# Performance work log

Measured on AMD Instinct MI355X. Metric: run time of the kernel, lower is better.

## Reference

```python
import jax, jax.numpy as jnp
import numpy as np

B, N_NODES, D, H, L, DFF, K = 16, 512, 256, 8, 4, 1024, 128
DH = D // H


def setup_inputs() -> dict:
    key = jax.random.key(0)
    ks = jax.random.split(key, 16)
    x = jax.random.normal(ks[0], (B, N_NODES, D), jnp.float32)
    d = jax.random.uniform(ks[1], (B, N_NODES, N_NODES), jnp.float32)
    dist = 0.5 * (d + jnp.swapaxes(d, -1, -2))
    dist = dist * (1.0 - jnp.eye(N_NODES, dtype=jnp.float32))  # zero diagonal
    mask = jnp.ones((B, 1, N_NODES), dtype=bool)
    s = 0.02
    Wq = jax.random.normal(ks[2], (L, D, D), jnp.float32) * s
    Wk = jax.random.normal(ks[3], (L, D, D), jnp.float32) * s
    Wv = jax.random.normal(ks[4], (L, D, D), jnp.float32) * s
    Wo = jax.random.normal(ks[5], (L, D, D), jnp.float32) * s
    W1 = jax.random.normal(ks[6], (L, D, DFF), jnp.float32) * s
    W2 = jax.random.normal(ks[7], (L, DFF, D), jnp.float32) * s
    ln1_g = jnp.ones((L, D), jnp.float32)
    ln1_b = jnp.zeros((L, D), jnp.float32)
    ln2_g = jnp.ones((L, D), jnp.float32)
    ln2_b = jnp.zeros((L, D), jnp.float32)
    gamma = jnp.ones((D,), jnp.float32)
    beta = jnp.zeros((D,), jnp.float32)
    return dict(x=x, dist=dist, mask=mask, Wq=Wq, Wk=Wk, Wv=Wv, Wo=Wo, W1=W1, W2=W2,
                ln1_g=ln1_g, ln1_b=ln1_b, ln2_g=ln2_g, ln2_b=ln2_b, gamma=gamma, beta=beta)


def _ln(x, g, b, eps=1e-6):
    mu = jnp.mean(x, axis=-1, keepdims=True)
    var = jnp.mean((x - mu) ** 2, axis=-1, keepdims=True)
    return (x - mu) * jax.lax.rsqrt(var + eps) * g + b


def _afps(scores, dist, k):
    # scores: [H, n, n] attention probs; dist: [n, n]; mask assumed all-True.
    s = jnp.sum(jnp.mean(scores, axis=0), axis=-2)            # [n] column sums
    d = dist / jnp.max(dist) + (s / jnp.max(s))[:, None] * 0.1  # [n, n]
    n = d.shape[0]
    mind0 = d[:, 0]                                            # min dist to {0}
    sel0 = jnp.zeros((n,), bool).at[0].set(True)

    def body(carry, _):
        mind, sel = carry
        cand = jnp.where(sel, -jnp.inf, mind)  # exclude already-selected
        new = jnp.argmax(cand)
        return (jnp.minimum(mind, d[:, new]), sel.at[new].set(True)), new

    _, picks = jax.lax.scan(body, (mind0, sel0), None, length=k - 1)
    return jnp.concatenate([jnp.zeros((1,), picks.dtype), picks])  # [k]


def reference(x, dist, mask, Wq, Wk, Wv, Wo, W1, W2, ln1_g, ln1_b, ln2_g, ln2_b, gamma, beta):
    key_mask = mask[:, :, None, :]  # [B,1,1,n] broadcast over heads/queries
    inv_sqrt = np.float32(1.0 / np.sqrt(DH))
    scores = None
    for i in range(L):
        h = _ln(x, ln1_g[i], ln1_b[i])
        q = (h @ Wq[i]).reshape(B, N_NODES, H, DH).transpose(0, 2, 1, 3)
        kk = (h @ Wk[i]).reshape(B, N_NODES, H, DH).transpose(0, 2, 1, 3)
        v = (h @ Wv[i]).reshape(B, N_NODES, H, DH).transpose(0, 2, 1, 3)
        logits = jnp.einsum('bhqd,bhkd->bhqk', q, kk) * inv_sqrt - dist[:, None]
        logits = jnp.where(key_mask, logits, jnp.float32(-1e9))
        scores = jax.nn.softmax(logits, axis=-1)               # [B,H,n,n]
        attn = jnp.einsum('bhqk,bhkd->bhqd', scores, v)
        x = x + attn.transpose(0, 2, 1, 3).reshape(B, N_NODES, D) @ Wo[i]
        h2 = _ln(x, ln2_g[i], ln2_b[i])
        x = x + jax.nn.gelu(h2 @ W1[i]) @ W2[i]
    # AFPS index selection runs under no_grad in the original
    idx = jax.vmap(lambda sc, dd: _afps(sc, dd, K))(
        jax.lax.stop_gradient(scores), jax.lax.stop_gradient(dist))  # [B,K]
    pooled = jnp.mean(jnp.take_along_axis(x, idx[:, :, None], axis=1), axis=1)  # [B,D]
    return _ln(pooled, gamma, beta)
```

## Files before the change

### kernel.cpp

```cpp
#include <hip/hip_runtime.h>
#include <hip/hip_bf16.h>
#include <math.h>

#define BB 16
#define NN 512
#define DD 256
#define HH 8
#define LL 4
#define DFF 1024
#define KSEL 128
#define DH 32

typedef __attribute__((ext_vector_type(8))) short bf16x8v;
typedef __attribute__((ext_vector_type(4))) float f32x4v;

static const size_t X_B    = 0;
static const size_t QKVB_B = 8388608;
static const size_t VT_B   = 20971520;
static const size_t FFN_B  = 8388608;
static const size_t H_B    = 25165824;
static const size_t ATT_B  = 29360128;
static const size_t WQKV_B = 33554432;
static const size_t WO_B   = 35127296;
static const size_t W1T_B  = 35651584;
static const size_t W2T_B  = 37748736;
static const size_t S_B    = 39845888;
static const size_t MAXD_B = 39878656;
static const size_t IDX_B  = 39878720;

__device__ __forceinline__ float gelu_f(float x) {
  float x3 = x * x * x;
  return 0.5f * x * (1.f + tanhf(0.7978845608028654f * (x + 0.044715f * x3)));
}

__device__ __forceinline__ short bf16raw(float v) {
  __hip_bfloat16 h = __float2bfloat16(v);
  return *reinterpret_cast<short*>(&h);
}

__device__ __forceinline__ float blk_sum_256(float v, float* stmp) {
  #pragma unroll
  for (int o = 32; o > 0; o >>= 1) v += __shfl_down(v, o, 64);
  if ((threadIdx.x & 63) == 0) stmp[threadIdx.x >> 6] = v;
  __syncthreads();
  if (threadIdx.x == 0) stmp[0] = stmp[0] + stmp[1] + stmp[2] + stmp[3];
  __syncthreads();
  float r = stmp[0];
  __syncthreads();
  return r;
}

template <int CTRL>
__device__ __forceinline__ unsigned long long dpp_mov_u64(unsigned long long x) {
  int lo = __builtin_amdgcn_update_dpp(0, (int)(unsigned)x, CTRL, 0xf, 0xf, true);
  int hi = __builtin_amdgcn_update_dpp(0, (int)(unsigned)(x >> 32), CTRL, 0xf, 0xf, true);
  return ((unsigned long long)(unsigned)hi << 32) | (unsigned)lo;
}

__device__ __forceinline__ void merge_top2(unsigned long long& b1, unsigned long long& b2,
                                           unsigned long long n1, unsigned long long n2) {
  if (n1 > b1) {
    b2 = (b1 > n2) ? b1 : n2;
    b1 = n1;
  } else {
    b2 = (b2 > n1) ? b2 : n1;
  }
}


__global__ __launch_bounds__(256) void cast_weights_kernel(
    const float* __restrict__ Wq, const float* __restrict__ Wk,
    const float* __restrict__ Wv, const float* __restrict__ Wo,
    const float* __restrict__ W1, const float* __restrict__ W2,
    __hip_bfloat16* __restrict__ qkvT, __hip_bfloat16* __restrict__ WoT,
    __hip_bfloat16* __restrict__ W1T, __hip_bfloat16* __restrict__ W2T) {
  int i = blockIdx.x * 256 + threadIdx.x;
  if (i < 786432) {
    int l = i / 196608, r = i % 196608;
    int n = r >> 8, k = r & 255;
    const float* src = (n < 256) ? Wq : (n < 512 ? Wk : Wv);
    qkvT[i] = __float2bfloat16(src[l * 65536 + k * 256 + (n & 255)]);
  } else if (i < 1048576) {
    int j = i - 786432;
    int l = j >> 16, r = j & 65535;
    int n = r >> 8, k = r & 255;
    WoT[j] = __float2bfloat16(Wo[l * 65536 + k * 256 + n]);
  } else if (i < 2097152) {
    int j = i - 1048576;
    int l = j >> 18, r = j & 262143;
    int n = r >> 8, k = r & 255;
    W1T[j] = __float2bfloat16(W1[l * 262144 + k * 1024 + n]);
  } else {
    int j = i - 2097152;
    int l = j >> 18, r = j & 262143;
    int n = r >> 10, k = r & 1023;
    W2T[j] = __float2bfloat16(W2[l * 262144 + k * 256 + n]);
  }
}

__global__ __launch_bounds__(256) void ln_cast_kernel(const float* __restrict__ in,
                                                      const float* __restrict__ g,
                                                      const float* __restrict__ bb,
                                                      __hip_bfloat16* __restrict__ out) {
  const int tid = threadIdx.x;
  const int lane = tid & 63;
  const size_t row = (size_t)blockIdx.x * 4 + (tid >> 6);
  const float4 v = *(const float4*)(in + row * DD + lane * 4);
  float s1 = v.x + v.y + v.z + v.w;
  #pragma unroll
  for (int o = 32; o > 0; o >>= 1) s1 += __shfl_xor(s1, o, 64);
  const float mu = s1 * (1.f / DD);
  const float d0 = v.x - mu, d1 = v.y - mu, d2 = v.z - mu, d3 = v.w - mu;
  float s2 = d0 * d0 + d1 * d1 + d2 * d2 + d3 * d3;
  #pragma unroll
  for (int o = 32; o > 0; o >>= 1) s2 += __shfl_xor(s2, o, 64);
  const float rsig = rsqrtf(s2 * (1.f / DD) + 1e-6f);
  const float4 gg = *(const float4*)(g + lane * 4);
  const float4 bv = *(const float4*)(bb + lane * 4);
  short4 o;
  o.x = bf16raw(d0 * rsig * gg.x + bv.x);
  o.y = bf16raw(d1 * rsig * gg.y + bv.y);
  o.z = bf16raw(d2 * rsig * gg.z + bv.z);
  o.w = bf16raw(d3 * rsig * gg.w + bv.w);
  *(short4*)((short*)out + row * DD + lane * 4) = o;
}

template <int MODE>
__global__ __launch_bounds__(256) void mfma_gemm(const __hip_bfloat16* __restrict__ A,
                                                 const __hip_bfloat16* __restrict__ Bt,
                                                 void* __restrict__ Cv,
                                                 __hip_bfloat16* __restrict__ Vto,
                                                 int M, int N, int Kd) {
  __shared__ short As[64 * 40];
  __shared__ short Bs[64 * 40];
  const int tid = threadIdx.x;
  const int w = tid >> 6, lane = tid & 63;
  const int m16 = lane & 15, quad = lane >> 4;
  const int bm = blockIdx.y << 6, bn = blockIdx.x << 6;
  const int srow = tid >> 2, scol = (tid & 3) << 3;

  f32x4v acc[4];
  #pragma unroll
  for (int nt = 0; nt < 4; ++nt) acc[nt] = (f32x4v){0.f, 0.f, 0.f, 0.f};

  const short* Ag = (const short*)A;
  const short* Bg = (const short*)Bt;

  for (int k0 = 0; k0 < Kd; k0 += 32) {
    *(bf16x8v*)&As[srow * 40 + scol] =
        *(const bf16x8v*)(Ag + (size_t)(bm + srow) * Kd + k0 + scol);
    *(bf16x8v*)&Bs[srow * 40 + scol] =
        *(const bf16x8v*)(Bg + (size_t)(bn + srow) * Kd + k0 + scol);
    __syncthreads();
    bf16x8v af = *(bf16x8v*)&As[(w * 16 + m16) * 40 + (quad << 3)];
    #pragma unroll
    for (int nt = 0; nt < 4; ++nt) {
      bf16x8v bf = *(bf16x8v*)&Bs[(nt * 16 + m16) * 40 + (quad << 3)];
      acc[nt] = __builtin_amdgcn_mfma_f32_16x16x32_bf16(af, bf, acc[nt], 0, 0, 0);
    }
    __syncthreads();
  }

  const int erow = bm + w * 16 + quad * 4;
  #pragma unroll
  for (int nt = 0; nt < 4; ++nt) {
    int col = bn + nt * 16 + m16;
    if (MODE == 3) {
      if (col < 512) {
        #pragma unroll
        for (int r = 0; r < 4; ++r)
          ((__hip_bfloat16*)Cv)[(size_t)(erow + r) * 768 + col] =
              __float2bfloat16(acc[nt][r]);
      } else {
        short4 pk;
        pk.x = bf16raw(acc[nt][0]); pk.y = bf16raw(acc[nt][1]);
        pk.z = bf16raw(acc[nt][2]); pk.w = bf16raw(acc[nt][3]);
        int bb2 = erow >> 9, key = erow & 511, dim = col - 512;
        *(short4*)((short*)Vto + (size_t)bb2 * 131072 + (size_t)dim * 512 + key) = pk;
      }
    } else {
      #pragma unroll
      for (int r = 0; r < 4; ++r)
        ((__hip_bfloat16*)Cv)[(size_t)(erow + r) * N + col] =
            __float2bfloat16(gelu_f(acc[nt][r]));
    }
  }
}

__device__ __forceinline__ void gemm_res_body(const __hip_bfloat16* __restrict__ A,
                                              const __hip_bfloat16* __restrict__ Bt,
                                              const float* __restrict__ Res,
                                              float* __restrict__ C,
                                              int N, int Kd, int bm,
                                              short* As, short* Bs) {
  const int tid = threadIdx.x;
  const int w = tid >> 6, lane = tid & 63;
  const int m16 = lane & 15, quad = lane >> 4;
  const int bn = blockIdx.x << 6;
  const int srow = tid >> 2, scol = (tid & 3) << 3;

  f32x4v acc[4];
  #pragma unroll
  for (int nt = 0; nt < 4; ++nt) acc[nt] = (f32x4v){0.f, 0.f, 0.f, 0.f};

  const short* Ag = (const short*)A;
  const short* Bg = (const short*)Bt;

  for (int k0 = 0; k0 < Kd; k0 += 32) {
    *(bf16x8v*)&As[srow * 40 + scol] =
        *(const bf16x8v*)(Ag + (size_t)(bm + srow) * Kd + k0 + scol);
    *(bf16x8v*)&Bs[srow * 40 + scol] =
        *(const bf16x8v*)(Bg + (size_t)(bn + srow) * Kd + k0 + scol);
    __syncthreads();
    bf16x8v af = *(bf16x8v*)&As[(w * 16 + m16) * 40 + (quad << 3)];
    #pragma unroll
    for (int nt = 0; nt < 4; ++nt) {
      bf16x8v bf = *(bf16x8v*)&Bs[(nt * 16 + m16) * 40 + (quad << 3)];
      acc[nt] = __builtin_amdgcn_mfma_f32_16x16x32_bf16(af, bf, acc[nt], 0, 0, 0);
    }
    __syncthreads();
  }

  const int erow = bm + w * 16 + quad * 4;
  #pragma unroll
  for (int nt = 0; nt < 4; ++nt) {
    int col = bn + nt * 16 + m16;
    #pragma unroll
    for (int r = 0; r < 4; ++r) {
      size_t off = (size_t)(erow + r) * N + col;
      C[off] = acc[nt][r] + Res[off];
    }
  }
}

__global__ __launch_bounds__(256) void mfma_gemm_res(const __hip_bfloat16* __restrict__ A,
                                                     const __hip_bfloat16* __restrict__ Bt,
                                                     const float* __restrict__ Res,
                                                     float* __restrict__ C,
                                                     int N, int Kd) {
  __shared__ short As[64 * 40];
  __shared__ short Bs[64 * 40];
  gemm_res_body(A, Bt, Res, C, N, Kd, blockIdx.y << 6, As, Bs);
}

__device__ void afps_wave(int b, int lane,
                          const float* __restrict__ dist,
                          const float* __restrict__ s,
                          const unsigned int* __restrict__ maxd,
                          int* __restrict__ idx_out) {
  const float* db = dist + (size_t)b * NN * NN;

  float sv[8];
  float ms = 0.f;
  #pragma unroll
  for (int r = 0; r < 8; ++r) {
    sv[r] = s[b * NN + r * 64 + lane];
    ms = fmaxf(ms, sv[r]);
  }
  #pragma unroll
  for (int o = 32; o > 0; o >>= 1) ms = fmaxf(ms, __shfl_xor(ms, o, 64));

  const float invmaxd = 1.0f / __uint_as_float(maxd[b]);
  float sn[8], mind[8];
  #pragma unroll
  for (int r = 0; r < 8; ++r) {
    sn[r] = (sv[r] / ms) * 0.1f;
    mind[r] = db[r * 64 + lane] * invmaxd + sn[r];
  }
  unsigned selm = (lane == 0) ? 1u : 0u;
  if (lane == 0) idx_out[b * KSEL + 0] = 0;

  int specIdx = -1;
  float sreg[8];

  for (int it = 1; it < KSEL; ++it) {
    unsigned long long b1 = 0ull, b2 = 0ull;
    #pragma unroll
    for (int r = 0; r < 8; ++r) {
      unsigned long long pk =
          ((selm >> r) & 1u) ? 0ull
            : (((unsigned long long)__float_as_uint(mind[r])) << 32) |
              (unsigned)(511 - (r * 64 + lane));
      if (pk > b1) { b2 = b1; b1 = pk; }
      else if (pk > b2) b2 = pk;
    }
    { unsigned long long n1 = dpp_mov_u64<0x111>(b1), n2 = dpp_mov_u64<0x111>(b2); merge_top2(b1, b2, n1, n2); }
    { unsigned long long n1 = dpp_mov_u64<0x112>(b1), n2 = dpp_mov_u64<0x112>(b2); merge_top2(b1, b2, n1, n2); }
    { unsigned long long n1 = dpp_mov_u64<0x114>(b1), n2 = dpp_mov_u64<0x114>(b2); merge_top2(b1, b2, n1, n2); }
    { unsigned long long n1 = dpp_mov_u64<0x118>(b1), n2 = dpp_mov_u64<0x118>(b2); merge_top2(b1, b2, n1, n2); }
    { unsigned long long n1 = dpp_mov_u64<0x142>(b1), n2 = dpp_mov_u64<0x142>(b2); merge_top2(b1, b2, n1, n2); }
    { unsigned long long n1 = dpp_mov_u64<0x143>(b1), n2 = dpp_mov_u64<0x143>(b2); merge_top2(b1, b2, n1, n2); }
    const unsigned w1 = (unsigned)__builtin_amdgcn_readlane((int)(unsigned)b1, 63);
    const unsigned w2 = (unsigned)__builtin_amdgcn_readlane((int)(unsigned)b2, 63);
    const int nw = 511 - (int)(w1 & 0x1ffu);
    const int sec = 511 - (int)(w2 & 0x1ffu);

    float rowv[8];
    if (nw == specIdx) {
      #pragma unroll
      for (int r = 0; r < 8; ++r) rowv[r] = sreg[r];
    } else {
      const float* row = db + (size_t)nw * NN;
      #pragma unroll
      for (int r = 0; r < 8; ++r) rowv[r] = row[r * 64 + lane];
    }
    {
      const float* srow = db + (size_t)sec * NN;
      #pragma unroll
      for (int r = 0; r < 8; ++r) sreg[r] = srow[r * 64 + lane];
      specIdx = sec;
    }
    if (lane == (nw & 63)) selm |= 1u << (nw >> 6);
    if (lane == 0) idx_out[b * KSEL + it] = nw;
    #pragma unroll
    for (int r = 0; r < 8; ++r)
      mind[r] = fminf(mind[r], fmaf(rowv[r], invmaxd, sn[r]));
  }
}

__global__ __launch_bounds__(256) void wo_gemm_afps(const __hip_bfloat16* __restrict__ A,
                                                    const __hip_bfloat16* __restrict__ Bt,
                                                    const float* __restrict__ Res,
                                                    float* __restrict__ C,
                                                    const float* __restrict__ dist,
                                                    const float* __restrict__ s,
                                                    const unsigned int* __restrict__ maxd,
                                                    int* __restrict__ idx_out) {
  __shared__ short As[64 * 40];
  __shared__ short Bs[64 * 40];
  if (blockIdx.y == 0) {
    const int b = blockIdx.x * 4 + (threadIdx.x >> 6);
    afps_wave(b, threadIdx.x & 63, dist, s, maxd, idx_out);
    return;
  }
  gemm_res_body(A, Bt, Res, C, DD, 256, (blockIdx.y - 1) << 6, As, Bs);
}

__global__ __launch_bounds__(512) void attn_kernel(const __hip_bfloat16* __restrict__ qkvb,
                                                   const __hip_bfloat16* __restrict__ vt,
                                                   const float* __restrict__ dist,
                                                   __hip_bfloat16* __restrict__ outg,
                                                   float* __restrict__ s_acc,
                                                   int accum) {
  __shared__ float Pf[8][16 * 36];
  const int tid = threadIdx.x;
  const int h = tid >> 6, lane = tid & 63;
  const int m16 = lane & 15, quad = lane >> 4;
  const int b = blockIdx.y;
  const int qbase = blockIdx.x * 16;
  const float scale = 0.17677669529663687f;
  const f32x4v zero = {0.f, 0.f, 0.f, 0.f};

  const short* qkvs = (const short*)qkvb;
  const short* vts = (const short*)vt + (size_t)b * 131072;
  float* Pw = Pf[h];

  bf16x8v qf = *(const bf16x8v*)(qkvs + ((size_t)(b * NN + qbase + m16)) * 768 + h * 32 + (quad << 3));

  int drow[4];
  #pragma unroll
  for (int r = 0; r < 4; ++r) drow[r] = (b * NN + qbase + quad * 4 + r) * NN;

  f32x4v accO0 = zero, accO1 = zero;
  float laccL[4] = {0.f, 0.f, 0.f, 0.f};

  for (int t0 = 0; t0 < NN; t0 += 32) {
    bf16x8v kf0 = *(const bf16x8v*)(qkvs + ((size_t)(b * NN + t0 + m16)) * 768 + 256 + h * 32 + (quad << 3));
    bf16x8v kf1 = *(const bf16x8v*)(qkvs + ((size_t)(b * NN + t0 + 16 + m16)) * 768 + 256 + h * 32 + (quad << 3));
    f32x4v s0 = __builtin_amdgcn_mfma_f32_16x16x32_bf16(qf, kf0, zero, 0, 0, 0);
    f32x4v s1 = __builtin_amdgcn_mfma_f32_16x16x32_bf16(qf, kf1, zero, 0, 0, 0);
    #pragma unroll
    for (int r = 0; r < 4; ++r) {
      float e0 = __expf(fmaf(s0[r], scale, -dist[drow[r] + t0 + m16]));
      float e1 = __expf(fmaf(s1[r], scale, -dist[drow[r] + t0 + 16 + m16]));
      laccL[r] += e0 + e1;
      Pw[(quad * 4 + r) * 36 + m16] = e0;
      Pw[(quad * 4 + r) * 36 + 16 + m16] = e1;
    }
    bf16x8v pfr;
    {
      const float* pr = &Pw[m16 * 36 + (quad << 3)];
      float4 pa = *(const float4*)pr;
      float4 pb = *(const float4*)(pr + 4);
      pfr[0] = bf16raw(pa.x); pfr[1] = bf16raw(pa.y);
      pfr[2] = bf16raw(pa.z); pfr[3] = bf16raw(pa.w);
      pfr[4] = bf16raw(pb.x); pfr[5] = bf16raw(pb.y);
      pfr[6] = bf16raw(pb.z); pfr[7] = bf16raw(pb.w);
    }
    bf16x8v vf0 = *(const bf16x8v*)(vts + (size_t)(h * 32 + m16) * 512 + t0 + (quad << 3));
    bf16x8v vf1 = *(const bf16x8v*)(vts + (size_t)(h * 32 + 16 + m16) * 512 + t0 + (quad << 3));
    accO0 = __builtin_amdgcn_mfma_f32_16x16x32_bf16(pfr, vf0, accO0, 0, 0, 0);
    accO1 = __builtin_amdgcn_mfma_f32_16x16x32_bf16(pfr, vf1, accO1, 0, 0, 0);
  }

  float invl[4];
  #pragma unroll
  for (int r = 0; r < 4; ++r) {
    float t = laccL[r];
    t += __shfl_xor(t, 1, 64); t += __shfl_xor(t, 2, 64);
    t += __shfl_xor(t, 4, 64); t += __shfl_xor(t, 8, 64);
    invl[r] = 1.f / t;
  }

  #pragma unroll
  for (int r = 0; r < 4; ++r) {
    size_t orow = (size_t)(b * NN + qbase + quad * 4 + r) * DD + h * 32;
    outg[orow + m16] = __float2bfloat16(accO0[r] * invl[r]);
    outg[orow + 16 + m16] = __float2bfloat16(accO1[r] * invl[r]);
  }

  if (accum) {
    for (int t0 = 0; t0 < NN; t0 += 32) {
      bf16x8v kf0 = *(const bf16x8v*)(qkvs + ((size_t)(b * NN + t0 + m16)) * 768 + 256 + h * 32 + (quad << 3));
      bf16x8v kf1 = *(const bf16x8v*)(qkvs + ((size_t)(b * NN + t0 + 16 + m16)) * 768 + 256 + h * 32 + (quad << 3));
      f32x4v s0 = __builtin_amdgcn_mfma_f32_16x16x32_bf16(qf, kf0, zero, 0, 0, 0);
      f32x4v s1 = __builtin_amdgcn_mfma_f32_16x16x32_bf16(qf, kf1, zero, 0, 0, 0);
      float p0 = 0.f, p1 = 0.f;
      #pragma unroll
      for (int r = 0; r < 4; ++r) {
        p0 += __expf(fmaf(s0[r], scale, -dist[drow[r] + t0 + m16])) * invl[r];
        p1 += __expf(fmaf(s1[r], scale, -dist[drow[r] + t0 + 16 + m16])) * invl[r];
      }
      p0 += __shfl_xor(p0, 16, 64); p0 += __shfl_xor(p0, 32, 64);
      p1 += __shfl_xor(p1, 16, 64); p1 += __shfl_xor(p1, 32, 64);
      if (quad == 0) {
        atomicAdd(&s_acc[b * NN + t0 + m16], p0 * 0.125f);
        atomicAdd(&s_acc[b * NN + t0 + 16 + m16], p1 * 0.125f);
      }
    }
  }
}

__global__ __launch_bounds__(256) void maxd_kernel(const float* __restrict__ dist,
                                                   unsigned int* __restrict__ maxd) {
  const int b = blockIdx.y;
  const int tid = threadIdx.x;
  const float4* p = (const float4*)(dist + (size_t)b * NN * NN) +
                    blockIdx.x * 8192 + tid;
  float m = 0.f;
  #pragma unroll 8
  for (int i = 0; i < 32; ++i) {
    float4 v = p[i * 256];
    m = fmaxf(m, fmaxf(fmaxf(v.x, v.y), fmaxf(v.z, v.w)));
  }
  #pragma unroll
  for (int o = 32; o > 0; o >>= 1) m = fmaxf(m, __shfl_xor(m, o, 64));
  __shared__ float wm[4];
  if ((tid & 63) == 0) wm[tid >> 6] = m;
  __syncthreads();
  if (tid == 0) {
    float mm = fmaxf(fmaxf(wm[0], wm[1]), fmaxf(wm[2], wm[3]));
    atomicMax(&maxd[b], __float_as_uint(mm));
  }
}

__global__ __launch_bounds__(256) void pool_ln_kernel(const float* __restrict__ x,
                                                      const int* __restrict__ idx,
                                                      const float* __restrict__ gamma,
                                                      const float* __restrict__ beta,
                                                      float* __restrict__ out) {
  __shared__ float stmp[4];
  __shared__ int sIdx[KSEL];
  const int b = blockIdx.x;
  const int d = threadIdx.x;
  if (d < KSEL) sIdx[d] = idx[b * KSEL + d];
  __syncthreads();
  float acc = 0.f;
  #pragma unroll 4
  for (int kk = 0; kk < KSEL; ++kk)
    acc += x[((size_t)b * NN + sIdx[kk]) * DD + d];
  float p = acc * (1.0f / KSEL);
  float mu = blk_sum_256(p, stmp) * (1.0f / DD);
  float diff = p - mu;
  float var = blk_sum_256(diff * diff, stmp) * (1.0f / DD);
  out[b * DD + d] = diff * rsqrtf(var + 1e-6f) * gamma[d] + beta[d];
}

extern "C" void kernel_launch(void* const* d_in, const int* in_sizes, int n_in,
                              void* d_out, int out_size, void* d_ws, size_t ws_size,
                              hipStream_t stream) {
  (void)in_sizes; (void)n_in; (void)out_size; (void)ws_size;
  const float* x_in  = (const float*)d_in[0];
  const float* dist  = (const float*)d_in[1];
  const float* Wq    = (const float*)d_in[3];
  const float* Wk    = (const float*)d_in[4];
  const float* Wv    = (const float*)d_in[5];
  const float* Wo    = (const float*)d_in[6];
  const float* W1    = (const float*)d_in[7];
  const float* W2    = (const float*)d_in[8];
  const float* ln1_g = (const float*)d_in[9];
  const float* ln1_b = (const float*)d_in[10];
  const float* ln2_g = (const float*)d_in[11];
  const float* ln2_b = (const float*)d_in[12];
  const float* gamma = (const float*)d_in[13];
  const float* beta  = (const float*)d_in[14];

  char* wsb = (char*)d_ws;
  float* x              = (float*)(wsb + X_B);
  __hip_bfloat16* qkvb  = (__hip_bfloat16*)(wsb + QKVB_B);
  __hip_bfloat16* vtb   = (__hip_bfloat16*)(wsb + VT_B);
  __hip_bfloat16* ffn   = (__hip_bfloat16*)(wsb + FFN_B);
  __hip_bfloat16* hb    = (__hip_bfloat16*)(wsb + H_B);
  __hip_bfloat16* ab    = (__hip_bfloat16*)(wsb + ATT_B);
  __hip_bfloat16* WqkvT = (__hip_bfloat16*)(wsb + WQKV_B);
  __hip_bfloat16* WoT   = (__hip_bfloat16*)(wsb + WO_B);
  __hip_bfloat16* W1T   = (__hip_bfloat16*)(wsb + W1T_B);
  __hip_bfloat16* W2T   = (__hip_bfloat16*)(wsb + W2T_B);
  float* sbuf = (float*)(wsb + S_B);
  unsigned int* maxdb = (unsigned int*)(wsb + MAXD_B);
  int*   idxb = (int*)(wsb + IDX_B);
  float* out  = (float*)d_out;

  hipMemsetAsync(sbuf, 0, BB * NN * sizeof(float) + 64, stream);
  cast_weights_kernel<<<12288, 256, 0, stream>>>(Wq, Wk, Wv, Wo, W1, W2,
                                                 WqkvT, WoT, W1T, W2T);
  maxd_kernel<<<dim3(8, BB), 256, 0, stream>>>(dist, maxdb);

  const int M = BB * NN;
  dim3 gqkv(768 / 64, M / 64);
  dim3 go(DD / 64, M / 64);
  dim3 goA(DD / 64, M / 64 + 1);
  dim3 gf(DFF / 64, M / 64);
  dim3 ga(NN / 16, BB);

  for (int l = 0; l < LL; ++l) {
    const float* xsrc = (l == 0) ? x_in : x;
    ln_cast_kernel<<<M / 4, 256, 0, stream>>>(xsrc, ln1_g + l * DD, ln1_b + l * DD, hb);
    mfma_gemm<3><<<gqkv, 256, 0, stream>>>(hb, WqkvT + (size_t)l * 768 * 256,
                                           qkvb, vtb, M, 768, 256);
    attn_kernel<<<ga, 512, 0, stream>>>(qkvb, vtb, dist, ab, sbuf, (l == LL - 1) ? 1 : 0);
    if (l == LL - 1) {
      wo_gemm_afps<<<goA, 256, 0, stream>>>(ab, WoT + (size_t)l * 65536, xsrc, x,
                                            dist, sbuf, maxdb, idxb);
    } else {
      mfma_gemm_res<<<go, 256, 0, stream>>>(ab, WoT + (size_t)l * 65536, xsrc, x, DD, 256);
    }
    ln_cast_kernel<<<M / 4, 256, 0, stream>>>(x, ln2_g + l * DD, ln2_b + l * DD, hb);
    mfma_gemm<2><<<gf, 256, 0, stream>>>(hb, W1T + (size_t)l * 262144,
                                         ffn, nullptr, M, DFF, 256);
    mfma_gemm_res<<<go, 256, 0, stream>>>(ffn, W2T + (size_t)l * 262144, x, x, DD, 1024);
  }
  pool_ln_kernel<<<BB, 256, 0, stream>>>(x, idxb, gamma, beta, out);
}
```

Baseline: 649.5 us.

## Double GEMM k-step to 64 and spread AFPS over blocks with dist prefetch

All MFMA GEMM kernels now stage a 64-wide K slice per iteration (padded LDS rows of 72), issuing two MFMA k-steps per barrier pair. This halves the number of __syncthreads per tile at the cost of more LDS. The fused Wo/AFPS kernel now gives each batch its own block: one wave runs AFPS while the other three waves stream through that batch's dist matrix to warm the cache. A dummy conditional atomic keeps that read from being optimised away. The change relies on dist being reread through L2 by AFPS, and it adds extra memory traffic.

Result: slower. 691.9 us (+6.5%).

```diff
diff --git a/kernel.cpp b/kernel.cpp
--- a/kernel.cpp
+++ b/kernel.cpp
@@ -27,6 +27,7 @@
 static const size_t S_B    = 39845888;
 static const size_t MAXD_B = 39878656;
 static const size_t IDX_B  = 39878720;
+static const size_t DUMMY_B = 39886912;
 
 __device__ __forceinline__ float gelu_f(float x) {
   float x3 = x * x * x;
@@ -131,8 +132,8 @@
                                                  void* __restrict__ Cv,
                                                  __hip_bfloat16* __restrict__ Vto,
                                                  int M, int N, int Kd) {
-  __shared__ short As[64 * 40];
-  __shared__ short Bs[64 * 40];
+  __shared__ short As[64 * 72];
+  __shared__ short Bs[64 * 72];
   const int tid = threadIdx.x;
   const int w = tid >> 6, lane = tid & 63;
   const int m16 = lane & 15, quad = lane >> 4;
@@ -146,17 +147,22 @@
   const short* Ag = (const short*)A;
   const short* Bg = (const short*)Bt;
 
-  for (int k0 = 0; k0 < Kd; k0 += 32) {
-    *(bf16x8v*)&As[srow * 40 + scol] =
-        *(const bf16x8v*)(Ag + (size_t)(bm + srow) * Kd + k0 + scol);
-    *(bf16x8v*)&Bs[srow * 40 + scol] =
-        *(const bf16x8v*)(Bg + (size_t)(bn + srow) * Kd + k0 + scol);
+  for (int k0 = 0; k0 < Kd; k0 += 64) {
+    const short* Agr = Ag + (size_t)(bm + srow) * Kd + k0 + scol;
+    const short* Bgr = Bg + (size_t)(bn + srow) * Kd + k0 + scol;
+    *(bf16x8v*)&As[srow * 72 + scol]      = *(const bf16x8v*)Agr;
+    *(bf16x8v*)&As[srow * 72 + 32 + scol] = *(const bf16x8v*)(Agr + 32);
+    *(bf16x8v*)&Bs[srow * 72 + scol]      = *(const bf16x8v*)Bgr;
+    *(bf16x8v*)&Bs[srow * 72 + 32 + scol] = *(const bf16x8v*)(Bgr + 32);
     __syncthreads();
-    bf16x8v af = *(bf16x8v*)&As[(w * 16 + m16) * 40 + (quad << 3)];
     #pragma unroll
-    for (int nt = 0; nt < 4; ++nt) {
-      bf16x8v bf = *(bf16x8v*)&Bs[(nt * 16 + m16) * 40 + (quad << 3)];
-      acc[nt] = __builtin_amdgcn_mfma_f32_16x16x32_bf16(af, bf, acc[nt], 0, 0, 0);
+    for (int kt = 0; kt < 2; ++kt) {
+      bf16x8v af = *(bf16x8v*)&As[(w * 16 + m16) * 72 + (kt << 5) + (quad << 3)];
+      #pragma unroll
+      for (int nt = 0; nt < 4; ++nt) {
+        bf16x8v bf = *(bf16x8v*)&Bs[(nt * 16 + m16) * 72 + (kt << 5) + (quad << 3)];
+        acc[nt] = __builtin_amdgcn_mfma_f32_16x16x32_bf16(af, bf, acc[nt], 0, 0, 0);
+      }
     }
     __syncthreads();
   }
@@ -206,17 +212,22 @@
   const short* Ag = (const short*)A;
   const short* Bg = (const short*)Bt;
 
-  for (int k0 = 0; k0 < Kd; k0 += 32) {
-    *(bf16x8v*)&As[srow * 40 + scol] =
-        *(const bf16x8v*)(Ag + (size_t)(bm + srow) * Kd + k0 + scol);
-    *(bf16x8v*)&Bs[srow * 40 + scol] =
-        *(const bf16x8v*)(Bg + (size_t)(bn + srow) * Kd + k0 + scol);
+  for (int k0 = 0; k0 < Kd; k0 += 64) {
+    const short* Agr = Ag + (size_t)(bm + srow) * Kd + k0 + scol;
+    const short* Bgr = Bg + (size_t)(bn + srow) * Kd + k0 + scol;
+    *(bf16x8v*)&As[srow * 72 + scol]      = *(const bf16x8v*)Agr;
+    *(bf16x8v*)&As[srow * 72 + 32 + scol] = *(const bf16x8v*)(Agr + 32);
+    *(bf16x8v*)&Bs[srow * 72 + scol]      = *(const bf16x8v*)Bgr;
+    *(bf16x8v*)&Bs[srow * 72 + 32 + scol] = *(const bf16x8v*)(Bgr + 32);
     __syncthreads();
-    bf16x8v af = *(bf16x8v*)&As[(w * 16 + m16) * 40 + (quad << 3)];
     #pragma unroll
-    for (int nt = 0; nt < 4; ++nt) {
-      bf16x8v bf = *(bf16x8v*)&Bs[(nt * 16 + m16) * 40 + (quad << 3)];
-      acc[nt] = __builtin_amdgcn_mfma_f32_16x16x32_bf16(af, bf, acc[nt], 0, 0, 0);
+    for (int kt = 0; kt < 2; ++kt) {
+      bf16x8v af = *(bf16x8v*)&As[(w * 16 + m16) * 72 + (kt << 5) + (quad << 3)];
+      #pragma unroll
+      for (int nt = 0; nt < 4; ++nt) {
+        bf16x8v bf = *(bf16x8v*)&Bs[(nt * 16 + m16) * 72 + (kt << 5) + (quad << 3)];
+        acc[nt] = __builtin_amdgcn_mfma_f32_16x16x32_bf16(af, bf, acc[nt], 0, 0, 0);
+      }
     }
     __syncthreads();
   }
@@ -238,8 +249,8 @@
                                                      const float* __restrict__ Res,
                                                      float* __restrict__ C,
                                                      int N, int Kd) {
-  __shared__ short As[64 * 40];
-  __shared__ short Bs[64 * 40];
+  __shared__ short As[64 * 72];
+  __shared__ short Bs[64 * 72];
   gemm_res_body(A, Bt, Res, C, N, Kd, blockIdx.y << 6, As, Bs);
 }
 
@@ -325,15 +336,24 @@
                                                     const float* __restrict__ dist,
                                                     const float* __restrict__ s,
                                                     const unsigned int* __restrict__ maxd,
-                                                    int* __restrict__ idx_out) {
-  __shared__ short As[64 * 40];
-  __shared__ short Bs[64 * 40];
-  if (blockIdx.y == 0) {
-    const int b = blockIdx.x * 4 + (threadIdx.x >> 6);
-    afps_wave(b, threadIdx.x & 63, dist, s, maxd, idx_out);
+                                                    int* __restrict__ idx_out,
+                                                    float* __restrict__ dummy) {
+  __shared__ short As[64 * 72];
+  __shared__ short Bs[64 * 72];
+  if (blockIdx.y < 4) {
+    const int b = blockIdx.y * 4 + blockIdx.x;
+    const int wv = threadIdx.x >> 6, lane = threadIdx.x & 63;
+    if (wv == 0) {
+      afps_wave(b, lane, dist, s, maxd, idx_out);
+    } else {
+      const float4* p = (const float4*)(dist + (size_t)b * NN * NN);
+      float acc = 0.f;
+      for (int i = (wv - 1) * 64 + lane; i < 65536; i += 192) acc += p[i].x;
+      if (acc == 123.456789f) atomicAdd(dummy, 1.f);
+    }
     return;
   }
-  gemm_res_body(A, Bt, Res, C, DD, 256, (blockIdx.y - 1) << 6, As, Bs);
+  gemm_res_body(A, Bt, Res, C, DD, 256, (blockIdx.y - 4) << 6, As, Bs);
 }
 
 __global__ __launch_bounds__(512) void attn_kernel(const __hip_bfloat16* __restrict__ qkvb,
@@ -509,6 +529,7 @@
   float* sbuf = (float*)(wsb + S_B);
   unsigned int* maxdb = (unsigned int*)(wsb + MAXD_B);
   int*   idxb = (int*)(wsb + IDX_B);
+  float* dummy = (float*)(wsb + DUMMY_B);
   float* out  = (float*)d_out;
 
   hipMemsetAsync(sbuf, 0, BB * NN * sizeof(float) + 64, stream);
@@ -519,7 +540,7 @@
   const int M = BB * NN;
   dim3 gqkv(768 / 64, M / 64);
   dim3 go(DD / 64, M / 64);
-  dim3 goA(DD / 64, M / 64 + 1);
+  dim3 goA(DD / 64, M / 64 + 4);
   dim3 gf(DFF / 64, M / 64);
   dim3 ga(NN / 16, BB);
 
@@ -531,7 +552,7 @@
     attn_kernel<<<ga, 512, 0, stream>>>(qkvb, vtb, dist, ab, sbuf, (l == LL - 1) ? 1 : 0);
     if (l == LL - 1) {
       wo_gemm_afps<<<goA, 256, 0, stream>>>(ab, WoT + (size_t)l * 65536, xsrc, x,
-                                            dist, sbuf, maxdb, idxb);
+                                            dist, sbuf, maxdb, idxb, dummy);
     } else {
       mfma_gemm_res<<<go, 256, 0, stream>>>(ab, WoT + (size_t)l * 65536, xsrc, x, DD, 256);
     }
```

## Spread AFPS waves across blocks with L2 prefetch helpers; LDS-reduce column sums

Applied to the files above, without the earlier changes.

The fused Wo GEMM + AFPS kernel now gives each batch's AFPS wave its own block, using 16 blocks instead of 4. The other three waves in each block stream that batch's distance matrix to warm the cache for the serial selection loop, with a never-true dummy atomic to stop the compiler dropping the loads. In the attention kernel, per-column score sums are first combined with shared-memory atomics and then flushed once per column to global memory. This cuts global atomic traffic, at the cost of extra barriers and a little extra dead read bandwidth.

After: 632.2 us. 2.7% less time.

```diff
diff --git a/kernel.cpp b/kernel.cpp
--- a/kernel.cpp
+++ b/kernel.cpp
@@ -27,6 +27,7 @@
 static const size_t S_B    = 39845888;
 static const size_t MAXD_B = 39878656;
 static const size_t IDX_B  = 39878720;
+static const size_t DUMMY_B = 39886912;
 
 __device__ __forceinline__ float gelu_f(float x) {
   float x3 = x * x * x;
@@ -325,15 +326,24 @@
                                                     const float* __restrict__ dist,
                                                     const float* __restrict__ s,
                                                     const unsigned int* __restrict__ maxd,
-                                                    int* __restrict__ idx_out) {
+                                                    int* __restrict__ idx_out,
+                                                    float* __restrict__ dummy) {
   __shared__ short As[64 * 40];
   __shared__ short Bs[64 * 40];
-  if (blockIdx.y == 0) {
-    const int b = blockIdx.x * 4 + (threadIdx.x >> 6);
-    afps_wave(b, threadIdx.x & 63, dist, s, maxd, idx_out);
+  if (blockIdx.y < 4) {
+    const int b = blockIdx.y * 4 + blockIdx.x;
+    const int wv = threadIdx.x >> 6, lane = threadIdx.x & 63;
+    if (wv == 0) {
+      afps_wave(b, lane, dist, s, maxd, idx_out);
+    } else {
+      const float4* p = (const float4*)(dist + (size_t)b * NN * NN);
+      float acc = 0.f;
+      for (int i = (wv - 1) * 64 + lane; i < 65536; i += 192) acc += p[i].x;
+      if (acc == 123.456789f) atomicAdd(dummy, 1.f);
+    }
     return;
   }
-  gemm_res_body(A, Bt, Res, C, DD, 256, (blockIdx.y - 1) << 6, As, Bs);
+  gemm_res_body(A, Bt, Res, C, DD, 256, (blockIdx.y - 4) << 6, As, Bs);
 }
 
 __global__ __launch_bounds__(512) void attn_kernel(const __hip_bfloat16* __restrict__ qkvb,
@@ -410,6 +420,10 @@
   }
 
   if (accum) {
+    float* sAcc = &Pf[0][0];
+    __syncthreads();
+    sAcc[tid] = 0.f;
+    __syncthreads();
     for (int t0 = 0; t0 < NN; t0 += 32) {
       bf16x8v kf0 = *(const bf16x8v*)(qkvs + ((size_t)(b * NN + t0 + m16)) * 768 + 256 + h * 32 + (quad << 3));
       bf16x8v kf1 = *(const bf16x8v*)(qkvs + ((size_t)(b * NN + t0 + 16 + m16)) * 768 + 256 + h * 32 + (quad << 3));
@@ -424,10 +438,12 @@
       p0 += __shfl_xor(p0, 16, 64); p0 += __shfl_xor(p0, 32, 64);
       p1 += __shfl_xor(p1, 16, 64); p1 += __shfl_xor(p1, 32, 64);
       if (quad == 0) {
-        atomicAdd(&s_acc[b * NN + t0 + m16], p0 * 0.125f);
-        atomicAdd(&s_acc[b * NN + t0 + 16 + m16], p1 * 0.125f);
+        atomicAdd(&sAcc[t0 + m16], p0);
+        atomicAdd(&sAcc[t0 + 16 + m16], p1);
       }
     }
+    __syncthreads();
+    atomicAdd(&s_acc[b * NN + tid], sAcc[tid] * 0.125f);
   }
 }
 
@@ -509,6 +525,7 @@
   float* sbuf = (float*)(wsb + S_B);
   unsigned int* maxdb = (unsigned int*)(wsb + MAXD_B);
   int*   idxb = (int*)(wsb + IDX_B);
+  float* dummy = (float*)(wsb + DUMMY_B);
   float* out  = (float*)d_out;
 
   hipMemsetAsync(sbuf, 0, BB * NN * sizeof(float) + 64, stream);
@@ -519,7 +536,7 @@
   const int M = BB * NN;
   dim3 gqkv(768 / 64, M / 64);
   dim3 go(DD / 64, M / 64);
-  dim3 goA(DD / 64, M / 64 + 1);
+  dim3 goA(DD / 64, M / 64 + 4);
   dim3 gf(DFF / 64, M / 64);
   dim3 ga(NN / 16, BB);
 
@@ -531,7 +548,7 @@
     attn_kernel<<<ga, 512, 0, stream>>>(qkvb, vtb, dist, ab, sbuf, (l == LL - 1) ? 1 : 0);
     if (l == LL - 1) {
       wo_gemm_afps<<<goA, 256, 0, stream>>>(ab, WoT + (size_t)l * 65536, xsrc, x,
-                                            dist, sbuf, maxdb, idxb);
+                                            dist, sbuf, maxdb, idxb, dummy);
     } else {
       mfma_gemm_res<<<go, 256, 0, stream>>>(ab, WoT + (size_t)l * 65536, xsrc, x, DD, 256);
     }
```
